# Performance work log

Hardware: AMD Instinct MI355X
Metric: run time of the kernel (lower is better)

## Reference

```python
import jax, jax.numpy as jnp
import numpy as np

# Static config (matches init_kwargs / chosen shapes)
B, H, W, C, NH, WS, SS = 8, 56, 56, 1024, 32, 7, 3
N = WS * WS            # tokens per window = 49
HID = 4 * C            # mlp hidden dim
HEAD = C // NH         # 32
SCALE = HEAD ** -0.5


def _rel_pos_index():
    # Same construction as the torch buffer `relative_position_index`
    coords = np.stack(np.meshgrid(np.arange(WS), np.arange(WS), indexing='ij'))  # (2, WS, WS)
    cf = coords.reshape(2, -1)                                    # (2, N)
    rel = (cf[:, :, None] - cf[:, None, :]).transpose(1, 2, 0)    # (N, N, 2)
    rel = rel.copy()
    rel[:, :, 0] += WS - 1
    rel[:, :, 1] += WS - 1
    rel[:, :, 0] *= 2 * WS - 1
    return jnp.asarray(rel.sum(-1))                               # (N, N) int

RPI = _rel_pos_index()


def _shift_mask():
    # Standard Swin cyclic-shift attention mask (0 / -100) for Hp=H, Wp=W
    img = np.zeros((1, H, W, 1), dtype=np.float32)
    cnt = 0
    for hs in (slice(0, -WS), slice(-WS, -SS), slice(-SS, None)):
        for ws in (slice(0, -WS), slice(-WS, -SS), slice(-SS, None)):
            img[:, hs, ws, :] = cnt
            cnt += 1
    mw = img.reshape(1, H // WS, WS, W // WS, WS, 1).transpose(0, 1, 3, 2, 4, 5).reshape(-1, N)
    diff = mw[:, None, :] - mw[:, :, None]
    return jnp.asarray(np.where(diff != 0, -100.0, 0.0).astype(np.float32))  # (nW, N, N)


def _window_partition(t):
    # (B, H, W, D) -> (B*nW, N, D)
    d = t.shape[-1]
    t = t.reshape(B, H // WS, WS, W // WS, WS, d).transpose(0, 1, 3, 2, 4, 5)
    return t.reshape(-1, N, d)


def _window_reverse(w):
    # (B*nW, N, D) -> (B, H, W, D)
    d = w.shape[-1]
    w = w.reshape(B, H // WS, W // WS, WS, WS, d).transpose(0, 1, 3, 2, 4, 5)
    return w.reshape(B, H, W, d)


def _layernorm(t, g, b, eps=1e-5):
    mu = t.mean(-1, keepdims=True)
    var = ((t - mu) ** 2).mean(-1, keepdims=True)
    return (t - mu) * jax.lax.rsqrt(var + eps) * g + b


def setup_inputs() -> dict:
    key = jax.random.key(0)
    ks = jax.random.split(key, 16)
    s = 0.02
    return {
        'x': jax.random.normal(ks[0], (B, H * W, C), jnp.float32),
        'v': jax.random.normal(ks[1], (B, H, W, C), jnp.float32),
        'mask_matrix': _shift_mask(),
        'norm1_g': jnp.ones((C,), jnp.float32),
        'norm1_b': jnp.zeros((C,), jnp.float32),
        'qk_w': jax.random.normal(ks[2], (2 * C, C), jnp.float32) * s,
        'qk_b': jnp.zeros((2 * C,), jnp.float32),
        'rpb_table': jax.random.normal(ks[3], ((2 * WS - 1) ** 2, NH), jnp.float32) * s,
        'proj_w': jax.random.normal(ks[4], (C, C), jnp.float32) * s,
        'proj_b': jnp.zeros((C,), jnp.float32),
        'norm2_g': jnp.ones((C,), jnp.float32),
        'norm2_b': jnp.zeros((C,), jnp.float32),
        'fc1_w': jax.random.normal(ks[5], (HID, C), jnp.float32) * s,
        'fc1_b': jnp.zeros((HID,), jnp.float32),
        'fc2_w': jax.random.normal(ks[6], (C, HID), jnp.float32) * s,
        'fc2_b': jnp.zeros((C,), jnp.float32),
    }


def reference(x, v, mask_matrix, norm1_g, norm1_b, qk_w, qk_b, rpb_table,
              proj_w, proj_b, norm2_g, norm2_b, fc1_w, fc1_b, fc2_w, fc2_b):
    shortcut = x                                             # (B, L, C)
    xn = _layernorm(x, norm1_g, norm1_b).reshape(B, H, W, C)
    # H, W divisible by WS -> no padding. Cyclic shift (shift_size > 0).
    sx = jnp.roll(xn, (-SS, -SS), axis=(1, 2))
    sv = jnp.roll(v, (-SS, -SS), axis=(1, 2))
    xw = _window_partition(sx)                               # (B_, N, C)
    vw = _window_partition(sv)                               # (B_, N, C)
    B_ = xw.shape[0]
    # q, k projections
    qk = (xw @ qk_w.T + qk_b).reshape(B_, N, 2, NH, HEAD)
    q = qk[:, :, 0].transpose(0, 2, 1, 3) * SCALE            # (B_, h, N, d)
    k = qk[:, :, 1].transpose(0, 2, 1, 3)
    attn = jnp.einsum('bhnd,bhmd->bhnm', q, k)               # (B_, h, N, N)
    bias = rpb_table[RPI].transpose(2, 0, 1)                 # (h, N, N)
    attn = attn + bias[None]
    nW = mask_matrix.shape[0]
    attn = attn.reshape(B_ // nW, nW, NH, N, N) + mask_matrix[None, :, None]
    attn = jax.nn.softmax(attn.reshape(B_, NH, N, N), axis=-1)
    vh = vw.reshape(B_, N, NH, HEAD).transpose(0, 2, 1, 3)   # (B_, h, N, d)
    o = jnp.einsum('bhnm,bhmd->bhnd', attn, vh)
    o = o.transpose(0, 2, 1, 3).reshape(B_, N, C)
    o = o @ proj_w.T + proj_b
    # reverse windows and shift
    xr = _window_reverse(o)
    xr = jnp.roll(xr, (SS, SS), axis=(1, 2)).reshape(B, H * W, C)
    x = shortcut + xr                                        # residual (drop_path = 0)
    hdn = _layernorm(x, norm2_g, norm2_b)
    hdn = jax.nn.gelu(hdn @ fc1_w.T + fc1_b, approximate=False)
    hdn = hdn @ fc2_w.T + fc2_b
    return x + hdn
```

## Files before the change

### kernel.cpp

```cpp
#include <hip/hip_runtime.h>
#include <math.h>

typedef __attribute__((ext_vector_type(8))) short bf16x8;
typedef __attribute__((ext_vector_type(4))) short short4v;
typedef __attribute__((ext_vector_type(4))) float f32x4;

#define SCALE 0.17677669529663687f

__device__ __forceinline__ short f2bf(float f) {
  unsigned u = __builtin_bit_cast(unsigned, f);
  unsigned r = u + 0x7fffu + ((u >> 16) & 1u);
  return (short)(r >> 16);
}

__device__ __forceinline__ void gll16(const short* g, short* l) {
  __builtin_amdgcn_global_load_lds(
      (const __attribute__((address_space(1))) unsigned int*)g,
      (__attribute__((address_space(3))) unsigned int*)l, 16, 0, 0);
}

__global__ __launch_bounds__(256) void cast_qkw_kernel(const float* __restrict__ src,
                                                       short* __restrict__ dst) {
  size_t i = (size_t)blockIdx.x * 256 + threadIdx.x;
  f32x4 v = *(const f32x4*)(src + i * 4);
  float sc = (i * 4 < (size_t)1024 * 1024) ? SCALE : 1.0f;
  short4v o;
#pragma unroll
  for (int j = 0; j < 4; ++j) o[j] = f2bf(v[j] * sc);
  *(short4v*)(dst + i * 4) = o;
}

__global__ __launch_bounds__(256) void cast_kernel(const float* __restrict__ src,
                                                   short* __restrict__ dst) {
  size_t i = (size_t)blockIdx.x * 256 + threadIdx.x;
  f32x4 v = *(const f32x4*)(src + i * 4);
  short4v o;
#pragma unroll
  for (int j = 0; j < 4; ++j) o[j] = f2bf(v[j]);
  *(short4v*)(dst + i * 4) = o;
}

__global__ __launch_bounds__(256) void ln1_permute_kernel(
    const float* __restrict__ x,
    const float* __restrict__ g1, const float* __restrict__ b1,
    short* __restrict__ xnw) {
  int r = blockIdx.x;
  int b = r / 3136, rem = r % 3136;
  int wi = rem / 49, n = rem % 49;
  int hs = (wi >> 3) * 7 + n / 7, wsf = (wi & 7) * 7 + n % 7;
  int ho = hs + 3; if (ho >= 56) ho -= 56;
  int wo = wsf + 3; if (wo >= 56) wo -= 56;
  size_t src = ((size_t)b * 3136 + ho * 56 + wo) * 1024;
  int t = threadIdx.x;
  f32x4 xv = *(const f32x4*)(x + src + t * 4);
  float s = xv[0] + xv[1] + xv[2] + xv[3];
  float s2 = xv[0] * xv[0] + xv[1] * xv[1] + xv[2] * xv[2] + xv[3] * xv[3];
#pragma unroll
  for (int m = 1; m < 64; m <<= 1) { s += __shfl_xor(s, m); s2 += __shfl_xor(s2, m); }
  __shared__ float red[8];
  int w = t >> 6;
  if ((t & 63) == 0) { red[w * 2] = s; red[w * 2 + 1] = s2; }
  __syncthreads();
  float ts = red[0] + red[2] + red[4] + red[6];
  float ts2 = red[1] + red[3] + red[5] + red[7];
  float mu = ts * (1.0f / 1024.0f);
  float var = ts2 * (1.0f / 1024.0f) - mu * mu;
  float rs = rsqrtf(var + 1e-5f);
  short4v xo;
#pragma unroll
  for (int j = 0; j < 4; ++j) {
    int cc = t * 4 + j;
    xo[j] = f2bf((xv[j] - mu) * rs * g1[cc] + b1[cc]);
  }
  *(short4v*)(xnw + (size_t)r * 1024 + t * 4) = xo;
}

__global__ __launch_bounds__(256) void ln2_kernel(const float* __restrict__ x2,
                                                  const float* __restrict__ g2,
                                                  const float* __restrict__ b2,
                                                  short* __restrict__ xn2) {
  int r = blockIdx.x;
  size_t src = (size_t)r * 1024;
  int t = threadIdx.x;
  f32x4 xv = *(const f32x4*)(x2 + src + t * 4);
  float s = xv[0] + xv[1] + xv[2] + xv[3];
  float s2 = xv[0] * xv[0] + xv[1] * xv[1] + xv[2] * xv[2] + xv[3] * xv[3];
#pragma unroll
  for (int m = 1; m < 64; m <<= 1) { s += __shfl_xor(s, m); s2 += __shfl_xor(s2, m); }
  __shared__ float red[8];
  int w = t >> 6;
  if ((t & 63) == 0) { red[w * 2] = s; red[w * 2 + 1] = s2; }
  __syncthreads();
  float ts = red[0] + red[2] + red[4] + red[6];
  float ts2 = red[1] + red[3] + red[5] + red[7];
  float mu = ts * (1.0f / 1024.0f);
  float var = ts2 * (1.0f / 1024.0f) - mu * mu;
  float rs = rsqrtf(var + 1e-5f);
  short4v xo;
#pragma unroll
  for (int j = 0; j < 4; ++j) {
    int cc = t * 4 + j;
    xo[j] = f2bf((xv[j] - mu) * rs * g2[cc] + b2[cc]);
  }
  *(short4v*)(xn2 + src + t * 4) = xo;
}

template <int EPI>
__global__ __launch_bounds__(512, 2) void gemm5(const short* __restrict__ A,
                                                const short* __restrict__ Bt,
                                                const float* __restrict__ bias,
                                                const float* __restrict__ add0,
                                                void* __restrict__ out, int N, int K,
                                                int ntm, int ntot) {
  __shared__ __align__(16) short lds[65536];
  char* basec = (char*)lds;
  int t = threadIdx.x;
  int l = t & 63;
  int w = t >> 6;
  int wm = w >> 2, wn = w & 3;
  int g = l >> 4, c = l & 15;
  int G = gridDim.x;
  int orig = blockIdx.x;
  int q = G >> 3, rr8 = G & 7, xcd = orig & 7, idx = orig >> 3;
  int tau = (xcd < rr8 ? xcd * (q + 1) : rr8 * (q + 1) + (xcd - rr8) * q) + idx;
  int bx = tau % ntm, by = tau / ntm;
  int tauN = tau + G; if (tauN >= ntot) tauN = tau;
  int bxN = tauN % ntm, byN = tauN / ntm;
  const short* AbC = A + (size_t)bx * 256 * K;
  const short* BbC = Bt + (size_t)by * 256 * K;
  const short* AbN = A + (size_t)bxN * 256 * K;
  const short* BbN = Bt + (size_t)byN * 256 * K;
  int o0 = t * 16, o1 = 8192 + t * 16;
  int ol0 = o0 ^ (((o0 >> 9) & 1) << 5);
  int ol1 = o1 ^ (((o1 >> 9) & 1) << 5);
  size_t off0 = (size_t)(ol0 >> 6) * K + ((ol0 & 63) >> 1);
  size_t off1 = (size_t)(ol1 >> 6) * K + ((ol1 & 63) >> 1);
  int NT = K >> 5;
  int labA = (wm * 128 + c) * 64 + g * 16; labA ^= ((labA >> 9) & 1) << 5;
  int labB = (wn * 64 + c) * 64 + g * 16;  labB ^= ((labB >> 9) & 1) << 5;
  const char* pA = basec + labA;
  const char* pB = basec + 65536 + labB;

  f32x4 acc[8][4] = {};
  bf16x8 afX[8], bfX[4], afY[8], bfY[4];

#define STG(rr, rel_)                                                   \
  do {                                                                  \
    int rl = (rel_);                                                    \
    const short* bA = (rl < NT) ? AbC : AbN;                            \
    const short* bB = (rl < NT) ? BbC : BbN;                            \
    int tt = rl & (NT - 1);                                             \
    size_t kb = (size_t)tt * 32;                                        \
    short* rgA = (short*)(basec + (rr) * 16384);                        \
    short* rgB = (short*)(basec + 65536 + (rr) * 16384);                \
    gll16(bA + kb + off0, rgA + t * 8);                                 \
    gll16(bA + kb + off1, rgA + 4096 + t * 8);                          \
    gll16(bB + kb + off0, rgB + t * 8);                                 \
    gll16(bB + kb + off1, rgB + 4096 + t * 8);                          \
  } while (0)

#define DSR(SA, SBv, rr)                                                   \
  do {                                                                     \
    _Pragma("unroll") for (int m = 0; m < 8; ++m)                          \
      SA[m] = *(const bf16x8*)(pA + (rr) * 16384 + m * 1024);              \
    _Pragma("unroll") for (int nf = 0; nf < 4; ++nf)                       \
      SBv[nf] = *(const bf16x8*)(pB + (rr) * 16384 + nf * 1024);           \
  } while (0)

#define SB __builtin_amdgcn_sched_barrier(0)

#define PH(j, CA, CB, LA, LB)                                      \
  do {                                                             \
    SB;                                                            \
    __builtin_amdgcn_s_barrier();                                  \
    SB;                                                            \
    __builtin_amdgcn_s_setprio(1);                                 \
    _Pragma("unroll") for (int m = 0; m < 8; ++m)                  \
      _Pragma("unroll") for (int nf = 0; nf < 4; ++nf)             \
        acc[m][nf] = __builtin_amdgcn_mfma_f32_16x16x32_bf16(      \
            CA[m], CB[nf], acc[m][nf], 0, 0, 0);                   \
    __builtin_amdgcn_s_setprio(0);                                 \
    SB;                                                            \
    DSR(LA, LB, ((j) + 1) & 3);                                    \
    SB;                                                            \
    STG(((j) + 3) & 3, s + (j) + 3);                               \
    asm volatile("s_waitcnt vmcnt(4)" ::: "memory");                \
    SB;                                                            \
  } while (0)

  STG(0, 0);
  STG(1, 1);
  STG(2, 2);
  asm volatile("s_waitcnt vmcnt(4)" ::: "memory");
  SB;
  __builtin_amdgcn_s_barrier();
  SB;
  DSR(afX, bfX, 0);

  while (true) {
    for (int s = 0; s < NT; s += 4) {
      PH(0, afX, bfX, afY, bfY);
      PH(1, afY, bfY, afX, bfX);
      PH(2, afX, bfX, afY, bfY);
      PH(3, afY, bfY, afX, bfX);
    }
    {
      int mb = bx * 256 + wm * 128;
      int nb = by * 256 + wn * 64;
#pragma unroll
      for (int m = 0; m < 8; ++m) {
#pragma unroll
        for (int i = 0; i < 4; ++i) {
          int row = mb + m * 16 + g * 4 + i;
          size_t orow = row;
          if (EPI == 1) {
            int bb = row / 3136, rem = row % 3136;
            int wi = rem / 49, n = rem % 49;
            int hs = (wi >> 3) * 7 + n / 7, wf = (wi & 7) * 7 + n % 7;
            int ho = hs + 3; if (ho >= 56) ho -= 56;
            int wo = wf + 3; if (wo >= 56) wo -= 56;
            orow = (size_t)bb * 3136 + ho * 56 + wo;
          }
#pragma unroll
          for (int nf = 0; nf < 4; ++nf) {
            int col = nb + nf * 16 + c;
            float val = acc[m][nf][i];
            if (EPI == 0) {
              float bv = bias[col] * (col < 1024 ? SCALE : 1.0f);
              ((short*)out)[(size_t)row * N + col] = f2bf(val + bv);
            } else if (EPI == 1) {
              ((float*)out)[orow * 1024 + col] = val + bias[col] + add0[orow * 1024 + col];
            } else if (EPI == 2) {
              float hv = val + bias[col];
              float z2 = 1.5957691216f * hv * (1.0f + 0.044715f * hv * hv);
              float th = 1.0f - 2.0f / (__expf(z2) + 1.0f);
              ((short*)out)[(size_t)row * N + col] = f2bf(0.5f * hv * (1.0f + th));
            } else {
              float res = add0[(size_t)row * 1024 + col];
              ((float*)out)[(size_t)row * 1024 + col] = val + bias[col] + res;
            }
          }
        }
      }
    }
    tau += G;
    if (tau >= ntot) break;
    bx = bxN; by = byN; AbC = AbN; BbC = BbN;
    int tau2 = tau + G; if (tau2 >= ntot) tau2 = tau;
    bxN = tau2 % ntm; byN = tau2 / ntm;
    AbN = A + (size_t)bxN * 256 * K;
    BbN = Bt + (size_t)byN * 256 * K;
#pragma unroll
    for (int m = 0; m < 8; ++m)
#pragma unroll
      for (int nf = 0; nf < 4; ++nf)
#pragma unroll
        for (int i = 0; i < 4; ++i) acc[m][nf][i] = 0.0f;
  }
#undef PH
#undef SB
#undef DSR
#undef STG
}

__global__ __launch_bounds__(256) void attn_kernel(const short* __restrict__ qk,
                                                   const float* __restrict__ v,
                                                   const float* __restrict__ rpb,
                                                   short* __restrict__ ao) {
  __shared__ __align__(16) float rpbt[32 * 169];
  __shared__ int cnt[49];
  __shared__ __align__(16) short Vt[4][32 * 72];
  __shared__ __align__(16) short Pl[4][64 * 72];
  int t = threadIdx.x, l = t & 63, w = t >> 6;
  int win = blockIdx.x >> 3;
  int h = (blockIdx.x & 7) * 4 + w;
  for (int e = t; e < 169 * 32; e += 256) {
    int hh = e / 169, idx = e - hh * 169;
    rpbt[e] = rpb[idx * 32 + hh];
  }
  if (t < 49) {
    int wi = win & 63;
    int hs = (wi >> 3) * 7 + t / 7, wsf = (wi & 7) * 7 + t % 7;
    int rh = hs < 49 ? 0 : (hs < 53 ? 1 : 2);
    int rw = wsf < 49 ? 0 : (wsf < 53 ? 1 : 2);
    cnt[t] = rh * 3 + rw;
  }
  if (l < 49) {
    int wi = win & 63, b = win >> 6;
    int hs = (wi >> 3) * 7 + l / 7, wsf = (wi & 7) * 7 + l % 7;
    int ho = hs + 3; if (ho >= 56) ho -= 56;
    int wo = wsf + 3; if (wo >= 56) wo -= 56;
    const float* vp = v + ((size_t)b * 3136 + ho * 56 + wo) * 1024 + h * 32;
#pragma unroll
    for (int d4 = 0; d4 < 8; ++d4) {
      f32x4 vv = *(const f32x4*)(vp + d4 * 4);
#pragma unroll
      for (int j = 0; j < 4; ++j) Vt[w][(d4 * 4 + j) * 72 + l] = f2bf(vv[j]);
    }
  } else {
#pragma unroll
    for (int d = 0; d < 32; ++d) Vt[w][d * 72 + l] = 0;
  }
  __syncthreads();
  int g = l >> 4, c = l & 15;
  bf16x8 qf[4], kf[4];
#pragma unroll
  for (int mt = 0; mt < 4; ++mt) {
    int r = mt * 16 + c; if (r > 48) r = 48;
    qf[mt] = *(const bf16x8*)&qk[((size_t)win * 49 + r) * 2048 + h * 32 + g * 8];
  }
#pragma unroll
  for (int nt = 0; nt < 4; ++nt) {
    int j = nt * 16 + c; if (j > 48) j = 48;
    kf[nt] = *(const bf16x8*)&qk[((size_t)win * 49 + j) * 2048 + 1024 + h * 32 + g * 8];
  }
  f32x4 s[4][4] = {};
#pragma unroll
  for (int mt = 0; mt < 4; ++mt)
#pragma unroll
    for (int nt = 0; nt < 4; ++nt)
      s[mt][nt] = __builtin_amdgcn_mfma_f32_16x16x32_bf16(qf[mt], kf[nt], s[mt][nt], 0, 0, 0);
#pragma unroll
  for (int mt = 0; mt < 4; ++mt)
#pragma unroll
    for (int nt = 0; nt < 4; ++nt)
#pragma unroll
      for (int i = 0; i < 4; ++i) {
        int r = mt * 16 + g * 4 + i;
        int j = nt * 16 + c;
        float val = s[mt][nt][i];
        if (r < 49 && j < 49) {
          int idx = (r / 7 - j / 7 + 6) * 13 + (r % 7 - j % 7 + 6);
          val += rpbt[h * 169 + idx];
          if (cnt[r] != cnt[j]) val -= 100.0f;
        } else {
          val = -1e30f;
        }
        s[mt][nt][i] = val;
      }
#pragma unroll
  for (int mt = 0; mt < 4; ++mt)
#pragma unroll
    for (int i = 0; i < 4; ++i) {
      float mx = s[mt][0][i];
#pragma unroll
      for (int nt = 1; nt < 4; ++nt) mx = fmaxf(mx, s[mt][nt][i]);
#pragma unroll
      for (int m2 = 1; m2 < 16; m2 <<= 1) mx = fmaxf(mx, __shfl_xor(mx, m2));
      float sum = 0.0f;
#pragma unroll
      for (int nt = 0; nt < 4; ++nt) {
        float e = __expf(s[mt][nt][i] - mx);
        s[mt][nt][i] = e;
        sum += e;
      }
#pragma unroll
      for (int m2 = 1; m2 < 16; m2 <<= 1) sum += __shfl_xor(sum, m2);
      float inv = 1.0f / sum;
#pragma unroll
      for (int nt = 0; nt < 4; ++nt) s[mt][nt][i] *= inv;
    }
#pragma unroll
  for (int mt = 0; mt < 4; ++mt)
#pragma unroll
    for (int nt = 0; nt < 4; ++nt)
#pragma unroll
      for (int i = 0; i < 4; ++i) {
        int r = mt * 16 + g * 4 + i, j = nt * 16 + c;
        Pl[w][r * 72 + j] = f2bf(s[mt][nt][i]);
      }
  __syncthreads();
  f32x4 o[4][2] = {};
#pragma unroll
  for (int kk = 0; kk < 2; ++kk) {
    bf16x8 vb[2];
#pragma unroll
    for (int n2 = 0; n2 < 2; ++n2)
      vb[n2] = *(const bf16x8*)&Vt[w][(n2 * 16 + c) * 72 + kk * 32 + g * 8];
#pragma unroll
    for (int mt = 0; mt < 4; ++mt) {
      bf16x8 pa = *(const bf16x8*)&Pl[w][(mt * 16 + c) * 72 + kk * 32 + g * 8];
#pragma unroll
      for (int n2 = 0; n2 < 2; ++n2)
        o[mt][n2] = __builtin_amdgcn_mfma_f32_16x16x32_bf16(pa, vb[n2], o[mt][n2], 0, 0, 0);
    }
  }
#pragma unroll
  for (int mt = 0; mt < 4; ++mt)
#pragma unroll
    for (int n2 = 0; n2 < 2; ++n2)
#pragma unroll
      for (int i = 0; i < 4; ++i) {
        int r = mt * 16 + g * 4 + i;
        if (r < 49) {
          int d = n2 * 16 + c;
          ao[((size_t)win * 49 + r) * 1024 + h * 32 + d] = f2bf(o[mt][n2][i]);
        }
      }
}

extern "C" void kernel_launch(void* const* d_in, const int* in_sizes, int n_in,
                              void* d_out, int out_size, void* d_ws, size_t ws_size,
                              hipStream_t stream) {
  (void)in_sizes; (void)n_in; (void)out_size; (void)ws_size;
  const float* x = (const float*)d_in[0];
  const float* v = (const float*)d_in[1];
  const float* n1g = (const float*)d_in[3];
  const float* n1b = (const float*)d_in[4];
  const float* qkw = (const float*)d_in[5];
  const float* qkb = (const float*)d_in[6];
  const float* rpb = (const float*)d_in[7];
  const float* pjw = (const float*)d_in[8];
  const float* pjb = (const float*)d_in[9];
  const float* n2g = (const float*)d_in[10];
  const float* n2b = (const float*)d_in[11];
  const float* f1w = (const float*)d_in[12];
  const float* f1b = (const float*)d_in[13];
  const float* f2w = (const float*)d_in[14];
  const float* f2b = (const float*)d_in[15];
  char* ws = (char*)d_ws;
  short* w_qk = (short*)(ws + 0);
  short* w_pj = (short*)(ws + 4194304);
  short* w_f1 = (short*)(ws + 6291456);
  short* w_f2 = (short*)(ws + 14680064);
  short* xnw  = (short*)(ws + 23068672);
  short* qkbuf= (short*)(ws + 74448896);
  short* aob  = (short*)(ws + 23068672);
  short* xn2  = (short*)(ws + 23068672);
  short* h1   = (short*)(ws + 74448896);
  float* out = (float*)d_out;

  cast_qkw_kernel<<<2048, 256, 0, stream>>>(qkw, w_qk);
  cast_kernel<<<1024, 256, 0, stream>>>(pjw, w_pj);
  cast_kernel<<<4096, 256, 0, stream>>>(f1w, w_f1);
  cast_kernel<<<4096, 256, 0, stream>>>(f2w, w_f2);
  ln1_permute_kernel<<<25088, 256, 0, stream>>>(x, n1g, n1b, xnw);
  gemm5<0><<<256, 512, 0, stream>>>(xnw, w_qk, qkb, nullptr, qkbuf, 2048, 1024, 98, 784);
  attn_kernel<<<4096, 256, 0, stream>>>(qkbuf, v, rpb, aob);
  gemm5<1><<<256, 512, 0, stream>>>(aob, w_pj, pjb, x, out, 1024, 1024, 98, 392);
  ln2_kernel<<<25088, 256, 0, stream>>>(out, n2g, n2b, xn2);
  for (int ch = 0; ch < 2; ++ch) {
    const short* a1 = xn2 + (size_t)ch * 12544 * 1024;
    float* o2 = out + (size_t)ch * 12544 * 1024;
    gemm5<2><<<256, 512, 0, stream>>>(a1, w_f1, f1b, nullptr, h1, 4096, 1024, 49, 784);
    gemm5<3><<<196, 512, 0, stream>>>(h1, w_f2, f2b, o2, o2, 1024, 4096, 49, 196);
  }
}
```

Baseline: 1.208 ms.

## Load GEMM B fragments directly from global into registers, halving LDS

The GEMM stops staging the weight (B) tile through LDS. Each wave now reads its B fragments straight from global memory into registers, one k-step ahead. Only the A tile goes through LDS, now triple-buffered at depth 2 instead of 3, so LDS use drops from 128KB to 64KB. The MFMA block is split into two halves so the second half can overlap the remaining A reads from LDS. The aim is to cut LDS traffic and footprint, at the cost of uncoalesced per-wave global loads for B, redundant B reads across the wm waves, and a shallower prefetch.

```diff
diff --git a/kernel.cpp b/kernel.cpp
--- a/kernel.cpp
+++ b/kernel.cpp
@@ -106,13 +106,13 @@
 }
 
 template <int EPI>
-__global__ __launch_bounds__(512, 2) void gemm5(const short* __restrict__ A,
+__global__ __launch_bounds__(512, 2) void gemm6(const short* __restrict__ A,
                                                 const short* __restrict__ Bt,
                                                 const float* __restrict__ bias,
                                                 const float* __restrict__ add0,
                                                 void* __restrict__ out, int N, int K,
                                                 int ntm, int ntot) {
-  __shared__ __align__(16) short lds[65536];
+  __shared__ __align__(16) short lds[32768];
   char* basec = (char*)lds;
   int t = threadIdx.x;
   int l = t & 63;
@@ -137,72 +137,78 @@
   size_t off1 = (size_t)(ol1 >> 6) * K + ((ol1 & 63) >> 1);
   int NT = K >> 5;
   int labA = (wm * 128 + c) * 64 + g * 16; labA ^= ((labA >> 9) & 1) << 5;
-  int labB = (wn * 64 + c) * 64 + g * 16;  labB ^= ((labB >> 9) & 1) << 5;
   const char* pA = basec + labA;
-  const char* pB = basec + 65536 + labB;
+  size_t bRow = (size_t)(wn * 64 + c) * K + g * 8;
 
   f32x4 acc[8][4] = {};
-  bf16x8 afX[8], bfX[4], afY[8], bfY[4];
-
-#define STG(rr, rel_)                                                   \
+  bf16x8 af[8], bfX[4], bfY[4];
+
+#define STG_A(rr, rel_)                                                 \
   do {                                                                  \
     int rl = (rel_);                                                    \
     const short* bA = (rl < NT) ? AbC : AbN;                            \
-    const short* bB = (rl < NT) ? BbC : BbN;                            \
-    int tt = rl & (NT - 1);                                             \
-    size_t kb = (size_t)tt * 32;                                        \
-    short* rgA = (short*)(basec + (rr) * 16384);                        \
-    short* rgB = (short*)(basec + 65536 + (rr) * 16384);                \
-    gll16(bA + kb + off0, rgA + t * 8);                                 \
-    gll16(bA + kb + off1, rgA + 4096 + t * 8);                          \
-    gll16(bB + kb + off0, rgB + t * 8);                                 \
-    gll16(bB + kb + off1, rgB + 4096 + t * 8);                          \
+    size_t kb = (size_t)(rl & (NT - 1)) * 32;                           \
+    short* rg = (short*)(basec + (rr) * 16384);                         \
+    gll16(bA + kb + off0, rg + t * 8);                                  \
+    gll16(bA + kb + off1, rg + 4096 + t * 8);                           \
   } while (0)
 
-#define DSR(SA, SBv, rr)                                                   \
-  do {                                                                     \
-    _Pragma("unroll") for (int m = 0; m < 8; ++m)                          \
-      SA[m] = *(const bf16x8*)(pA + (rr) * 16384 + m * 1024);              \
-    _Pragma("unroll") for (int nf = 0; nf < 4; ++nf)                       \
-      SBv[nf] = *(const bf16x8*)(pB + (rr) * 16384 + nf * 1024);           \
+#define BLOAD(SET, rel_)                                                \
+  do {                                                                  \
+    int rl = (rel_);                                                    \
+    const short* bse = (rl < NT) ? BbC : BbN;                           \
+    size_t kb = (size_t)(rl & (NT - 1)) * 32;                           \
+    _Pragma("unroll") for (int nf = 0; nf < 4; ++nf)                    \
+      SET[nf] = *(const bf16x8*)(bse + bRow + kb + (size_t)nf * 16 * K); \
   } while (0)
 
+#define DSR_A(rr)                                                       \
+  do {                                                                  \
+    _Pragma("unroll") for (int m = 0; m < 8; ++m)                       \
+      af[m] = *(const bf16x8*)(pA + (rr) * 16384 + m * 1024);           \
+  } while (0)
+
 #define SB __builtin_amdgcn_sched_barrier(0)
 
-#define PH(j, CA, CB, LA, LB)                                      \
+#define PH(j, CUR, NXT)                                            \
   do {                                                             \
+    BLOAD(NXT, s + (j) + 1);                                       \
+    STG_A(((j) + 2) & 3, s + (j) + 2);                             \
+    asm volatile("s_waitcnt vmcnt(6)" ::: "memory");               \
     SB;                                                            \
     __builtin_amdgcn_s_barrier();                                  \
     SB;                                                            \
+    DSR_A((j) & 3);                                                \
+    asm volatile("s_waitcnt lgkmcnt(4)" ::: "memory");             \
+    SB;                                                            \
     __builtin_amdgcn_s_setprio(1);                                 \
-    _Pragma("unroll") for (int m = 0; m < 8; ++m)                  \
+    _Pragma("unroll") for (int m = 0; m < 4; ++m)                  \
       _Pragma("unroll") for (int nf = 0; nf < 4; ++nf)             \
         acc[m][nf] = __builtin_amdgcn_mfma_f32_16x16x32_bf16(      \
-            CA[m], CB[nf], acc[m][nf], 0, 0, 0);                   \
+            af[m], CUR[nf], acc[m][nf], 0, 0, 0);                  \
     __builtin_amdgcn_s_setprio(0);                                 \
     SB;                                                            \
-    DSR(LA, LB, ((j) + 1) & 3);                                    \
-    SB;                                                            \
-    STG(((j) + 3) & 3, s + (j) + 3);                               \
-    asm volatile("s_waitcnt vmcnt(4)" ::: "memory");                \
+    asm volatile("s_waitcnt lgkmcnt(0)" ::: "memory");             \
+    SB;                                                            \
+    __builtin_amdgcn_s_setprio(1);                                 \
+    _Pragma("unroll") for (int m = 4; m < 8; ++m)                  \
+      _Pragma("unroll") for (int nf = 0; nf < 4; ++nf)             \
+        acc[m][nf] = __builtin_amdgcn_mfma_f32_16x16x32_bf16(      \
+            af[m], CUR[nf], acc[m][nf], 0, 0, 0);                  \
+    __builtin_amdgcn_s_setprio(0);                                 \
     SB;                                                            \
   } while (0)
 
-  STG(0, 0);
-  STG(1, 1);
-  STG(2, 2);
-  asm volatile("s_waitcnt vmcnt(4)" ::: "memory");
-  SB;
-  __builtin_amdgcn_s_barrier();
-  SB;
-  DSR(afX, bfX, 0);
+  BLOAD(bfX, 0);
+  STG_A(0, 0);
+  STG_A(1, 1);
 
   while (true) {
     for (int s = 0; s < NT; s += 4) {
-      PH(0, afX, bfX, afY, bfY);
-      PH(1, afY, bfY, afX, bfX);
-      PH(2, afX, bfX, afY, bfY);
-      PH(3, afY, bfY, afX, bfX);
+      PH(0, bfX, bfY);
+      PH(1, bfY, bfX);
+      PH(2, bfX, bfY);
+      PH(3, bfY, bfX);
     }
     {
       int mb = bx * 256 + wm * 128;
@@ -259,8 +265,9 @@
   }
 #undef PH
 #undef SB
-#undef DSR
-#undef STG
+#undef DSR_A
+#undef BLOAD
+#undef STG_A
 }
 
 __global__ __launch_bounds__(256) void attn_kernel(const short* __restrict__ qk,
@@ -435,14 +442,14 @@
   cast_kernel<<<4096, 256, 0, stream>>>(f1w, w_f1);
   cast_kernel<<<4096, 256, 0, stream>>>(f2w, w_f2);
   ln1_permute_kernel<<<25088, 256, 0, stream>>>(x, n1g, n1b, xnw);
-  gemm5<0><<<256, 512, 0, stream>>>(xnw, w_qk, qkb, nullptr, qkbuf, 2048, 1024, 98, 784);
+  gemm6<0><<<256, 512, 0, stream>>>(xnw, w_qk, qkb, nullptr, qkbuf, 2048, 1024, 98, 784);
   attn_kernel<<<4096, 256, 0, stream>>>(qkbuf, v, rpb, aob);
-  gemm5<1><<<256, 512, 0, stream>>>(aob, w_pj, pjb, x, out, 1024, 1024, 98, 392);
+  gemm6<1><<<256, 512, 0, stream>>>(aob, w_pj, pjb, x, out, 1024, 1024, 98, 392);
   ln2_kernel<<<25088, 256, 0, stream>>>(out, n2g, n2b, xn2);
   for (int ch = 0; ch < 2; ++ch) {
     const short* a1 = xn2 + (size_t)ch * 12544 * 1024;
     float* o2 = out + (size_t)ch * 12544 * 1024;
-    gemm5<2><<<256, 512, 0, stream>>>(a1, w_f1, f1b, nullptr, h1, 4096, 1024, 49, 784);
-    gemm5<3><<<196, 512, 0, stream>>>(h1, w_f2, f2b, o2, o2, 1024, 4096, 49, 196);
-  }
-}
+    gemm6<2><<<256, 512, 0, stream>>>(a1, w_f1, f1b, nullptr, h1, 4096, 1024, 49, 784);
+    gemm6<3><<<196, 512, 0, stream>>>(h1, w_f2, f2b, o2, o2, 1024, 4096, 49, 196);
+  }
+}
```

After: 1.226 ms. About the same (+1.4%).
